# Optimization experiments

Measured on AMD Instinct MI355X. Metric: run time of the kernel, lower is better.

Reference implementation:

```python
import jax, jax.numpy as jnp
import numpy as np

H = 1000   # hidden_size
B = 64     # batch
S = 512    # encoder source length


def setup_inputs() -> dict:
    key = jax.random.key(0)
    ks = jax.random.split(key, 9)
    scale = 0.02
    return {
        "decoder_hidden": jax.random.normal(ks[0], (1, B, H), jnp.float32),
        "context": jax.random.normal(ks[1], (B, S, 2 * H), jnp.float32),
        "mask": jax.random.randint(ks[2], (B, S, 1), 0, 2) == 1,
        "W_a": jax.random.normal(ks[3], (H, 2 * H), jnp.float32) * scale,
        "W_b": jax.random.normal(ks[4], (H, H), jnp.float32) * scale,
        "W_c_w": jax.random.normal(ks[5], (1, H), jnp.float32) * scale,
        "W_c_b": jax.random.normal(ks[6], (1,), jnp.float32) * scale,
        "dense_w": jax.random.normal(ks[7], (H, 2 * H), jnp.float32) * scale,
        "dense_b": jax.random.normal(ks[8], (H,), jnp.float32) * scale,
    }


def reference(decoder_hidden, context, mask, W_a, W_b, W_c_w, W_c_b, dense_w, dense_b):
    # context_in: (B, S, H)
    context_in = jnp.einsum('bsd,hd->bsh', context, W_a)
    # hidden_in: (1, B, H) @ W_b.T -> transpose(0,1) -> (B, 1, H)
    hidden_in = jnp.transpose(jnp.einsum('nbd,hd->nbh', decoder_hidden, W_b), (1, 0, 2))
    # scores: (B, S, 1)
    attention = jnp.einsum('bsh,oh->bso', jnp.tanh(context_in + hidden_in), W_c_w) + W_c_b
    attention = jnp.where(mask, jnp.asarray(-1e6, attention.dtype), attention)
    attention_softmaxed = jax.nn.softmax(attention, axis=1)  # softmax over source length
    # weighted_sum: (B, 1, S) x (B, S, 2H) -> (B, 1, 2H)
    weighted_sum = jnp.einsum('bso,bsd->bod', attention_softmaxed, context)
    # dense: (B, 1, H)
    return jnp.einsum('bod,hd->boh', weighted_sum, dense_w) + dense_b
```

## Files before the change

### kernel.cpp

```cpp
#include <hip/hip_runtime.h>
#include <hip/hip_bf16.h>

#define H 1000
#define B 64
#define S 512
#define D 2000
#define KP 2048
#define NP 1024
#define MP 32768
#define KS 10

typedef __attribute__((ext_vector_type(8))) short short8;
typedef __attribute__((ext_vector_type(4))) float f32x4;

__device__ inline unsigned short f2bf(float f) {
  __hip_bfloat16 h = __float2bfloat16(f);
  union { __hip_bfloat16 h; unsigned short u; } c; c.h = h;
  return c.u;
}
__device__ inline float bf2f(unsigned short u) {
  union { unsigned u; float f; } x; x.u = ((unsigned)u) << 16;
  return x.f;
}

__global__ __launch_bounds__(256) void k_dect(const float* __restrict__ dec,
                                              float* __restrict__ dec_t) {
  const int d = blockIdx.x * 4 + (threadIdx.x >> 6);
  const int b = threadIdx.x & 63;
  dec_t[d * 64 + b] = dec[b * H + d];
}

__global__ __launch_bounds__(256) void k_hidden2(const float* __restrict__ dec_t,
                                                 const float* __restrict__ Wb,
                                                 float* __restrict__ hi) {
  const int h = blockIdx.x * 4 + (threadIdx.x >> 6);
  const int lane = threadIdx.x & 63;
  const float* w = Wb + (size_t)h * H;
  float acc = 0.f;
#pragma unroll 4
  for (int d = 0; d < H; ++d) acc += w[d] * dec_t[d * 64 + lane];
  hi[lane * H + h] = acc;
}

__global__ __launch_bounds__(256) void k_hidden(const float* __restrict__ dec,
                                                const float* __restrict__ Wb,
                                                float* __restrict__ hi) {
  __shared__ float sdec[H];
  const int b = blockIdx.y;
  const int h = blockIdx.x * 4 + (threadIdx.x >> 6);
  const int lane = threadIdx.x & 63;
  for (int d = threadIdx.x; d < H; d += 256) sdec[d] = dec[b * H + d];
  __syncthreads();
  const float* w = Wb + (size_t)h * H;
  float acc = 0.f;
  for (int d = lane; d < H; d += 64) acc += w[d] * sdec[d];
  for (int o = 32; o; o >>= 1) acc += __shfl_xor(acc, o);
  if (lane == 0) hi[b * H + h] = acc;
}

__global__ __launch_bounds__(256) void k_cvt_t(const float* __restrict__ src,
                                               unsigned short* __restrict__ dst,
                                               int valid_rows) {
  __shared__ unsigned short st[2][4096];
  const int rp = blockIdx.x;
  const int tid = threadIdx.x;
  const int row = tid >> 2;
  const int kq = tid & 3;

#define CVT_BODY(T, P)                                                          \
  do {                                                                          \
    const int t = (T);                                                          \
    unsigned short v[2][8];                                                     \
    _Pragma("unroll")                                                           \
    for (int w = 0; w < 2; ++w) {                                               \
      const int r = row + w * 64;                                               \
      const int grow = rp * 128 + r;                                            \
      const int gcol = t * 32 + kq * 8;                                         \
      if (grow < valid_rows && gcol + 8 <= D) {                                 \
        const float* p = src + (size_t)grow * D + gcol;                         \
        float4 x = *(const float4*)p;                                           \
        float4 y = *(const float4*)(p + 4);                                     \
        v[w][0] = f2bf(x.x); v[w][1] = f2bf(x.y); v[w][2] = f2bf(x.z);          \
        v[w][3] = f2bf(x.w); v[w][4] = f2bf(y.x); v[w][5] = f2bf(y.y);          \
        v[w][6] = f2bf(y.z); v[w][7] = f2bf(y.w);                               \
      } else {                                                                  \
        _Pragma("unroll")                                                       \
        for (int z = 0; z < 8; ++z) v[w][z] = 0;                                \
      }                                                                         \
    }                                                                           \
    *(short8*)&st[P][(kq * 128 + row) * 8] = *(short8*)&v[0][0];                \
    *(short8*)&st[P][(kq * 128 + row + 64) * 8] = *(short8*)&v[1][0];           \
    __syncthreads();                                                            \
    unsigned short* ob = dst + ((size_t)rp * 64 + t) * 4096;                    \
    *(short8*)(ob + tid * 8) = *(short8*)&st[P][tid * 8];                       \
    *(short8*)(ob + 2048 + tid * 8) = *(short8*)&st[P][2048 + tid * 8];         \
  } while (0)

  const int t0 = blockIdx.y * 16;
  for (int tt = 0; tt < 16; tt += 2) {
    CVT_BODY(t0 + tt, 0);
    CVT_BODY(t0 + tt + 1, 1);
  }
#undef CVT_BODY
}

__global__ __launch_bounds__(256) void k_scores_fast(const unsigned short* __restrict__ ctxb,
                                                     const unsigned short* __restrict__ wab,
                                                     const float* __restrict__ hi,
                                                     const float* __restrict__ Wcw,
                                                     float* __restrict__ scores) {
  __shared__ unsigned short As[3][4096];
  __shared__ unsigned short Bs[3][4096];

  const int bid = blockIdx.x;
  const int swz = (bid & 7) * 256 + (bid >> 3);
  const int rtile = swz >> 3;
  const int ctile = swz & 7;
  const int row0 = rtile * 128;
  const int col0 = ctile * 128;

  const int tid = threadIdx.x;
  const int lane = tid & 63;
  const int wid = tid >> 6;
  const int wm = wid >> 1, wn = wid & 1;
  const int fr = lane & 15, fq = lane >> 4;

  const unsigned short* ga = ctxb + (size_t)rtile * (64 * 4096);
  const unsigned short* gb = wab + (size_t)ctile * (64 * 4096);

  f32x4 acc[4][4];
#pragma unroll
  for (int i = 0; i < 4; ++i)
#pragma unroll
    for (int j = 0; j < 4; ++j) acc[i][j] = (f32x4){0.f, 0.f, 0.f, 0.f};

#define STAGE(T, BUF)                                                                                      \
  do {                                                                                                     \
    const unsigned short* pa = ga + (size_t)(T) * 4096 + tid * 8;                                          \
    const unsigned short* pb = gb + (size_t)(T) * 4096 + tid * 8;                                          \
    __builtin_amdgcn_global_load_lds((const __attribute__((address_space(1))) unsigned int*)pa,            \
                                     (__attribute__((address_space(3))) unsigned int*)&As[BUF][tid * 8],   \
                                     16, 0, 0);                                                            \
    __builtin_amdgcn_global_load_lds((const __attribute__((address_space(1))) unsigned int*)(pa + 2048),   \
                                     (__attribute__((address_space(3))) unsigned int*)&As[BUF][tid * 8 + 2048], \
                                     16, 0, 0);                                                            \
    __builtin_amdgcn_global_load_lds((const __attribute__((address_space(1))) unsigned int*)pb,            \
                                     (__attribute__((address_space(3))) unsigned int*)&Bs[BUF][tid * 8],   \
                                     16, 0, 0);                                                            \
    __builtin_amdgcn_global_load_lds((const __attribute__((address_space(1))) unsigned int*)(pb + 2048),   \
                                     (__attribute__((address_space(3))) unsigned int*)&Bs[BUF][tid * 8 + 2048], \
                                     16, 0, 0);                                                            \
  } while (0)

  const int aoff = fq * 1024 + (wm * 64 + fr) * 8;
  const int boff = fq * 1024 + (wn * 64 + fr) * 8;

#define COMPUTE(BI)                                                                     \
  do {                                                                                  \
    short8 a[4], bb[4];                                                                 \
    _Pragma("unroll")                                                                   \
    for (int mi = 0; mi < 4; ++mi) a[mi] = *(const short8*)&As[BI][aoff + mi * 128];    \
    _Pragma("unroll")                                                                   \
    for (int ni = 0; ni < 4; ++ni) bb[ni] = *(const short8*)&Bs[BI][boff + ni * 128];   \
    __builtin_amdgcn_s_setprio(1);                                                      \
    _Pragma("unroll")                                                                   \
    for (int mi = 0; mi < 4; ++mi)                                                      \
      _Pragma("unroll")                                                                 \
      for (int ni = 0; ni < 4; ++ni)                                                    \
        acc[mi][ni] = __builtin_amdgcn_mfma_f32_16x16x32_bf16(a[mi], bb[ni], acc[mi][ni], 0, 0, 0); \
    __builtin_amdgcn_s_setprio(0);                                                      \
  } while (0)

#define ITER(T, BC, BS)                                      \
  do {                                                       \
    STAGE((T) + 2, BS);                                      \
    COMPUTE(BC);                                             \
    asm volatile("s_waitcnt vmcnt(4)" ::: "memory");         \
    __builtin_amdgcn_s_barrier();                            \
  } while (0)

  STAGE(0, 0);
  STAGE(1, 1);
  asm volatile("s_waitcnt vmcnt(4)" ::: "memory");
  __builtin_amdgcn_s_barrier();

  for (int t = 0; t < 60; t += 3) {
    ITER(t, 0, 2);
    ITER(t + 1, 1, 0);
    ITER(t + 2, 2, 1);
  }
  ITER(60, 0, 2);
  ITER(61, 1, 0);
  COMPUTE(2);
  asm volatile("s_waitcnt vmcnt(0)" ::: "memory");
  __builtin_amdgcn_s_barrier();
  COMPUTE(0);
#undef ITER
#undef STAGE
#undef COMPUTE

  const int b_idx = row0 >> 9;
  float wcv[4], hiv[4];
#pragma unroll
  for (int ni = 0; ni < 4; ++ni) {
    const int h = col0 + wn * 64 + ni * 16 + fr;
    wcv[ni] = (h < H) ? Wcw[h] : 0.f;
    hiv[ni] = (h < H) ? hi[b_idx * H + h] : 0.f;
  }
#pragma unroll
  for (int mi = 0; mi < 4; ++mi) {
#pragma unroll
    for (int r = 0; r < 4; ++r) {
      float p = 0.f;
#pragma unroll
      for (int ni = 0; ni < 4; ++ni)
        p += wcv[ni] * tanhf(acc[mi][ni][r] + hiv[ni]);
      p += __shfl_xor(p, 1);
      p += __shfl_xor(p, 2);
      p += __shfl_xor(p, 4);
      p += __shfl_xor(p, 8);
      if (fr == 0)
        atomicAdd(&scores[row0 + wm * 64 + mi * 16 + fq * 4 + r], p);
    }
  }
}

#define BM 128
#define BN 128
#define BK 32
#define NT 63
__global__ __launch_bounds__(256) void k_scores(const float* __restrict__ ctx,
                                                const float* __restrict__ Wa,
                                                const float* __restrict__ hi,
                                                const float* __restrict__ Wcw,
                                                float* __restrict__ scores) {
  __shared__ unsigned short As[2][BM][BK];
  __shared__ unsigned short Bs[2][BN][BK];

  const int bid = blockIdx.x;
  const int swz = (bid & 7) * 256 + (bid >> 3);
  const int row0 = (swz >> 3) * BM;
  const int col0 = (swz & 7) * BN;

  const int tid = threadIdx.x;
  const int lane = tid & 63;
  const int wid = tid >> 6;
  const int wm = wid >> 1;
  const int wn = wid & 1;
  const int fr = lane & 15;
  const int fq = lane >> 4;

  const int trow = tid >> 1;
  const int thalf = tid & 1;

  f32x4 acc[4][4];
#pragma unroll
  for (int i = 0; i < 4; ++i)
#pragma unroll
    for (int j = 0; j < 4; ++j) acc[i][j] = (f32x4){0.f, 0.f, 0.f, 0.f};

  const float* aptr = ctx + (size_t)(row0 + trow) * D + thalf * 16;
  const int hB = col0 + trow;
  const bool bvalid = (hB < H);
  const float* bptr = Wa + (size_t)(bvalid ? hB : 0) * D + thalf * 16;

  float4 ra[4], rb[4];

#define LOADT(T)                                                     \
  do {                                                               \
    const int base = (T) * BK + thalf * 16;                          \
    _Pragma("unroll")                                                \
    for (int q = 0; q < 4; ++q) {                                    \
      const int kk = base + q * 4;                                   \
      if (kk < D) {                                                  \
        ra[q] = *(const float4*)(aptr + (T) * BK + q * 4);           \
        if (bvalid) rb[q] = *(const float4*)(bptr + (T) * BK + q * 4); \
      }                                                              \
    }                                                                \
  } while (0)

#define CVTW(T, BUF)                                                 \
  do {                                                               \
    const int base = (T) * BK + thalf * 16;                          \
    unsigned short ta[16], tb[16];                                   \
    _Pragma("unroll")                                                \
    for (int q = 0; q < 4; ++q) {                                    \
      const int kk = base + q * 4;                                   \
      const bool v = (kk < D);                                       \
      ta[q * 4 + 0] = v ? f2bf(ra[q].x) : 0;                         \
      ta[q * 4 + 1] = v ? f2bf(ra[q].y) : 0;                         \
      ta[q * 4 + 2] = v ? f2bf(ra[q].z) : 0;                         \
      ta[q * 4 + 3] = v ? f2bf(ra[q].w) : 0;                         \
      const bool vb = v && bvalid;                                   \
      tb[q * 4 + 0] = vb ? f2bf(rb[q].x) : 0;                        \
      tb[q * 4 + 1] = vb ? f2bf(rb[q].y) : 0;                        \
      tb[q * 4 + 2] = vb ? f2bf(rb[q].z) : 0;                        \
      tb[q * 4 + 3] = vb ? f2bf(rb[q].w) : 0;                        \
    }                                                                \
    *(short8*)&As[BUF][trow][thalf * 16]     = *(short8*)&ta[0];     \
    *(short8*)&As[BUF][trow][thalf * 16 + 8] = *(short8*)&ta[8];     \
    *(short8*)&Bs[BUF][trow][thalf * 16]     = *(short8*)&tb[0];     \
    *(short8*)&Bs[BUF][trow][thalf * 16 + 8] = *(short8*)&tb[8];     \
  } while (0)

  LOADT(0);
  CVTW(0, 0);
  LOADT(1);
  __syncthreads();

  int cur = 0;
  for (int t = 0; t < NT; ++t) {
    short8 a[4], bbf[4];
#pragma unroll
    for (int mi = 0; mi < 4; ++mi)
      a[mi] = *(const short8*)&As[cur][wm * 64 + mi * 16 + fr][fq * 8];
#pragma unroll
    for (int ni = 0; ni < 4; ++ni)
      bbf[ni] = *(const short8*)&Bs[cur][wn * 64 + ni * 16 + fr][fq * 8];
#pragma unroll
    for (int mi = 0; mi < 4; ++mi)
#pragma unroll
      for (int ni = 0; ni < 4; ++ni)
        acc[mi][ni] = __builtin_amdgcn_mfma_f32_16x16x32_bf16(a[mi], bbf[ni], acc[mi][ni], 0, 0, 0);

    if (t + 1 < NT) {
      CVTW(t + 1, cur ^ 1);
      if (t + 2 < NT) LOADT(t + 2);
    }
    __syncthreads();
    cur ^= 1;
  }
#undef LOADT
#undef CVTW

  const int b_idx = row0 >> 9;
  float wcv[4], hiv[4];
#pragma unroll
  for (int ni = 0; ni < 4; ++ni) {
    const int h = col0 + wn * 64 + ni * 16 + fr;
    wcv[ni] = (h < H) ? Wcw[h] : 0.f;
    hiv[ni] = (h < H) ? hi[b_idx * H + h] : 0.f;
  }
#pragma unroll
  for (int mi = 0; mi < 4; ++mi) {
#pragma unroll
    for (int r = 0; r < 4; ++r) {
      float p = 0.f;
#pragma unroll
      for (int ni = 0; ni < 4; ++ni)
        p += wcv[ni] * tanhf(acc[mi][ni][r] + hiv[ni]);
      p += __shfl_xor(p, 1);
      p += __shfl_xor(p, 2);
      p += __shfl_xor(p, 4);
      p += __shfl_xor(p, 8);
      if (fr == 0)
        atomicAdd(&scores[row0 + wm * 64 + mi * 16 + fq * 4 + r], p);
    }
  }
}

__global__ __launch_bounds__(256) void k_softmax(const float* __restrict__ scores,
                                                 const int* __restrict__ mask,
                                                 const float* __restrict__ Wcb,
                                                 float* __restrict__ probs) {
  __shared__ float buf[S];
  __shared__ float rbuf[256];
  const int b = blockIdx.x;
  const float bias = Wcb[0];
  float mx = -3.4e38f;
  for (int s = threadIdx.x; s < S; s += 256) {
    float a = mask[b * S + s] ? -1e6f : (scores[b * S + s] + bias);
    buf[s] = a;
    mx = fmaxf(mx, a);
  }
  rbuf[threadIdx.x] = mx;
  __syncthreads();
  for (int w = 128; w > 0; w >>= 1) {
    if (threadIdx.x < w) rbuf[threadIdx.x] = fmaxf(rbuf[threadIdx.x], rbuf[threadIdx.x + w]);
    __syncthreads();
  }
  mx = rbuf[0];
  __syncthreads();
  float sum = 0.f;
  for (int s = threadIdx.x; s < S; s += 256) {
    float e = expf(buf[s] - mx);
    buf[s] = e;
    sum += e;
  }
  rbuf[threadIdx.x] = sum;
  __syncthreads();
  for (int w = 128; w > 0; w >>= 1) {
    if (threadIdx.x < w) rbuf[threadIdx.x] += rbuf[threadIdx.x + w];
    __syncthreads();
  }
  const float inv = 1.f / rbuf[0];
  for (int s = threadIdx.x; s < S; s += 256) probs[b * S + s] = buf[s] * inv;
}

__global__ __launch_bounds__(256) void k_wsum_b(const unsigned short* __restrict__ ctxb,
                                                const float* __restrict__ probs,
                                                float* __restrict__ ws2) {
  __shared__ float sp[S];
  const int t = blockIdx.x;
  const int b = blockIdx.y;
  const int tid = threadIdx.x;
  const int kq = tid >> 6;
  const int lane = tid & 63;
  for (int i = tid; i < S; i += 256) sp[i] = probs[b * S + i];
  __syncthreads();
  float acc[8];
#pragma unroll
  for (int e = 0; e < 8; ++e) acc[e] = 0.f;
#pragma unroll
  for (int rp4 = 0; rp4 < 4; ++rp4) {
    const unsigned short* chunk = ctxb + ((size_t)(b * 4 + rp4) * 64 + t) * 4096;
#pragma unroll
    for (int w = 0; w < 2; ++w) {
      const int row = lane + w * 64;
      short8 v = *(const short8*)&chunk[(kq * 128 + row) * 8];
      const float pv = sp[rp4 * 128 + row];
#pragma unroll
      for (int e = 0; e < 8; ++e) acc[e] += pv * bf2f((unsigned short)v[e]);
    }
  }
#pragma unroll
  for (int o = 32; o; o >>= 1)
#pragma unroll
    for (int e = 0; e < 8; ++e) acc[e] += __shfl_xor(acc[e], o);
  const int d0 = t * 32 + kq * 8;
  if (lane == 0 && d0 < D) {
#pragma unroll
    for (int e = 0; e < 8; ++e) ws2[(size_t)b * D + d0 + e] = acc[e];
  }
}

__global__ __launch_bounds__(256) void k_wsum(const float* __restrict__ ctx,
                                              const float* __restrict__ probs,
                                              float* __restrict__ ws2) {
  __shared__ float p[S];
  const int b = blockIdx.y;
  const int d = blockIdx.x * 256 + threadIdx.x;
  for (int s = threadIdx.x; s < S; s += 256) p[s] = probs[b * S + s];
  __syncthreads();
  if (d < D) {
    float acc = 0.f;
    for (int s = 0; s < S; ++s) acc += p[s] * ctx[(size_t)(b * S + s) * D + d];
    ws2[b * D + d] = acc;
  }
}

__global__ __launch_bounds__(256) void k_dense_part(const float* __restrict__ ws2,
                                                    const float* __restrict__ Dw,
                                                    float* __restrict__ partial) {
  __shared__ float sw[64][201];
  const int tid = threadIdx.x;
  const int ks = blockIdx.y;
  const int k0 = ks * 200;
  for (int idx = tid; idx < 64 * 200; idx += 256) {
    const int b = idx / 200, k = idx - b * 200;
    sw[b][k] = ws2[(size_t)b * D + k0 + k];
  }
  __syncthreads();
  const int h = blockIdx.x * 4 + (tid >> 6);
  const int lane = tid & 63;
  const float* wrow = Dw + (size_t)h * D + k0;
  float acc = 0.f;
#pragma unroll 8
  for (int k = 0; k < 200; ++k) acc += wrow[k] * sw[lane][k];
  partial[((size_t)ks * 64 + lane) * 1000 + h] = acc;
}

__global__ __launch_bounds__(256) void k_dense_red(const float* __restrict__ partial,
                                                   const float* __restrict__ Db,
                                                   float* __restrict__ out) {
  const int idx = blockIdx.x * 256 + threadIdx.x;
  const int h = idx % 1000;
  float acc = Db[h];
#pragma unroll
  for (int ks = 0; ks < KS; ++ks) acc += partial[(size_t)ks * 64000 + idx];
  out[idx] = acc;
}

__global__ __launch_bounds__(256) void k_dense(const float* __restrict__ ws2,
                                               const float* __restrict__ Dw,
                                               const float* __restrict__ Db,
                                               float* __restrict__ out) {
  __shared__ float v[D];
  const int b = blockIdx.y;
  const int h = blockIdx.x * 256 + threadIdx.x;
  for (int d = threadIdx.x; d < D; d += 256) v[d] = ws2[b * D + d];
  __syncthreads();
  if (h < H) {
    const float* w = Dw + (size_t)h * D;
    float acc = 0.f;
    for (int d = 0; d < D; ++d) acc += w[d] * v[d];
    out[b * H + h] = acc + Db[h];
  }
}

extern "C" void kernel_launch(void* const* d_in, const int* in_sizes, int n_in,
                              void* d_out, int out_size, void* d_ws, size_t ws_size,
                              hipStream_t stream) {
  const float* dec = (const float*)d_in[0];
  const float* ctx = (const float*)d_in[1];
  const int*   mask = (const int*)d_in[2];
  const float* Wa  = (const float*)d_in[3];
  const float* Wb  = (const float*)d_in[4];
  const float* Wcw = (const float*)d_in[5];
  const float* Wcb = (const float*)d_in[6];
  const float* Dw  = (const float*)d_in[7];
  const float* Db  = (const float*)d_in[8];
  float* out = (float*)d_out;

  float* hi     = (float*)d_ws;
  float* scores = hi + B * H;
  float* probs  = scores + B * S;
  float* ws2    = probs + B * S;
  const size_t float_words = (size_t)B * H + 2 * B * S + B * D;
  unsigned short* ctx_b = (unsigned short*)((float*)d_ws + float_words);
  unsigned short* wa_b  = ctx_b + (size_t)MP * KP;
  float* dec_t  = (float*)ctx_b;
  float* partial = (float*)ctx_b;
  const size_t need = float_words * 4 + ((size_t)MP * KP + (size_t)NP * KP) * 2;

  hipMemsetAsync(scores, 0, B * S * sizeof(float), stream);
  if (ws_size >= need) {
    k_dect<<<250, 256, 0, stream>>>(dec, dec_t);
    k_hidden2<<<250, 256, 0, stream>>>(dec_t, Wb, hi);
    k_cvt_t<<<dim3(MP / 128, 4), 256, 0, stream>>>(ctx, ctx_b, MP);
    k_cvt_t<<<dim3(NP / 128, 4), 256, 0, stream>>>(Wa, wa_b, H);
    k_scores_fast<<<2048, 256, 0, stream>>>(ctx_b, wa_b, hi, Wcw, scores);
    k_softmax<<<B, 256, 0, stream>>>(scores, mask, Wcb, probs);
    k_wsum_b<<<dim3(63, B), 256, 0, stream>>>(ctx_b, probs, ws2);
    k_dense_part<<<dim3(250, KS), 256, 0, stream>>>(ws2, Dw, partial);
    k_dense_red<<<250, 256, 0, stream>>>(partial, Db, out);
  } else {
    k_hidden<<<dim3(250, B), 256, 0, stream>>>(dec, Wb, hi);
    k_scores<<<2048, 256, 0, stream>>>(ctx, Wa, hi, Wcw, scores);
    k_softmax<<<B, 256, 0, stream>>>(scores, mask, Wcb, probs);
    k_wsum<<<dim3((D + 255) / 256, B), 256, 0, stream>>>(ctx, probs, ws2);
    k_dense<<<dim3((H + 255) / 256, B), 256, 0, stream>>>(ws2, Dw, Db, out);
  }
}
```

Before: 462.3 us.

## Enlarge scores GEMM tiles to 256x256 with 32x32 MFMA and fast tanh

The scores GEMM moves from 128x128 tiles with 4 waves to 256x256 tiles with 8 waves, using 32x32x16 bf16 MFMA instructions. The bf16 packed layout of context and W_a changes to 256-row chunks to match, and the conversion and weighted-sum kernels are updated to read it. This raises arithmetic intensity and reduces redundant global and LDS traffic per FLOP. It also swaps tanhf for an exp-based tanh. The cost is much larger LDS use (96KB) and more registers per thread, which lowers occupancy, and there are fewer blocks (512) to fill the CUs.

```diff
diff --git a/kernel.cpp b/kernel.cpp
--- a/kernel.cpp
+++ b/kernel.cpp
@@ -12,6 +12,7 @@
 
 typedef __attribute__((ext_vector_type(8))) short short8;
 typedef __attribute__((ext_vector_type(4))) float f32x4;
+typedef __attribute__((ext_vector_type(16))) float f32x16;
 
 __device__ inline unsigned short f2bf(float f) {
   __hip_bfloat16 h = __float2bfloat16(f);
@@ -21,6 +22,10 @@
 __device__ inline float bf2f(unsigned short u) {
   union { unsigned u; float f; } x; x.u = ((unsigned)u) << 16;
   return x.f;
+}
+__device__ inline float tanh_fast(float x) {
+  float e2 = __expf(2.f * x);
+  return 1.f - 2.f / (e2 + 1.f);
 }
 
 __global__ __launch_bounds__(256) void k_dect(const float* __restrict__ dec,
@@ -61,20 +66,19 @@
 __global__ __launch_bounds__(256) void k_cvt_t(const float* __restrict__ src,
                                                unsigned short* __restrict__ dst,
                                                int valid_rows) {
-  __shared__ unsigned short st[2][4096];
+  __shared__ unsigned short st[2][8192];
   const int rp = blockIdx.x;
   const int tid = threadIdx.x;
-  const int row = tid >> 2;
+  const int r0 = tid >> 2;
   const int kq = tid & 3;
 
 #define CVT_BODY(T, P)                                                          \
   do {                                                                          \
     const int t = (T);                                                          \
-    unsigned short v[2][8];                                                     \
+    unsigned short v[4][8];                                                     \
     _Pragma("unroll")                                                           \
-    for (int w = 0; w < 2; ++w) {                                               \
-      const int r = row + w * 64;                                               \
-      const int grow = rp * 128 + r;                                            \
+    for (int w = 0; w < 4; ++w) {                                               \
+      const int grow = rp * 256 + r0 + w * 64;                                  \
       const int gcol = t * 32 + kq * 8;                                         \
       if (grow < valid_rows && gcol + 8 <= D) {                                 \
         const float* p = src + (size_t)grow * D + gcol;                         \
@@ -88,87 +92,98 @@
         for (int z = 0; z < 8; ++z) v[w][z] = 0;                                \
       }                                                                         \
     }                                                                           \
-    *(short8*)&st[P][(kq * 128 + row) * 8] = *(short8*)&v[0][0];                \
-    *(short8*)&st[P][(kq * 128 + row + 64) * 8] = *(short8*)&v[1][0];           \
+    _Pragma("unroll")                                                           \
+    for (int w = 0; w < 4; ++w)                                                 \
+      *(short8*)&st[P][(kq * 256 + r0 + w * 64) * 8] = *(short8*)&v[w][0];      \
     __syncthreads();                                                            \
-    unsigned short* ob = dst + ((size_t)rp * 64 + t) * 4096;                    \
-    *(short8*)(ob + tid * 8) = *(short8*)&st[P][tid * 8];                       \
-    *(short8*)(ob + 2048 + tid * 8) = *(short8*)&st[P][2048 + tid * 8];         \
+    unsigned short* ob = dst + ((size_t)rp * 64 + t) * 8192;                    \
+    _Pragma("unroll")                                                           \
+    for (int s = 0; s < 4; ++s)                                                 \
+      *(short8*)(ob + (tid + s * 256) * 8) = *(short8*)&st[P][(tid + s * 256) * 8]; \
   } while (0)
 
-  const int t0 = blockIdx.y * 16;
-  for (int tt = 0; tt < 16; tt += 2) {
+  const int t0 = blockIdx.y * 8;
+  for (int tt = 0; tt < 8; tt += 2) {
     CVT_BODY(t0 + tt, 0);
     CVT_BODY(t0 + tt + 1, 1);
   }
 #undef CVT_BODY
 }
 
-__global__ __launch_bounds__(256) void k_scores_fast(const unsigned short* __restrict__ ctxb,
+__global__ __launch_bounds__(512) void k_scores_fast(const unsigned short* __restrict__ ctxb,
                                                      const unsigned short* __restrict__ wab,
                                                      const float* __restrict__ hi,
                                                      const float* __restrict__ Wcw,
                                                      float* __restrict__ scores) {
-  __shared__ unsigned short As[3][4096];
-  __shared__ unsigned short Bs[3][4096];
+  __shared__ unsigned short As[3][8192];
+  __shared__ unsigned short Bs[3][8192];
 
   const int bid = blockIdx.x;
-  const int swz = (bid & 7) * 256 + (bid >> 3);
-  const int rtile = swz >> 3;
-  const int ctile = swz & 7;
-  const int row0 = rtile * 128;
-  const int col0 = ctile * 128;
+  const int swz = (bid & 7) * 64 + (bid >> 3);
+  const int rtile = swz >> 2;
+  const int ctile = swz & 3;
+  const int row0 = rtile * 256;
+  const int col0 = ctile * 256;
 
   const int tid = threadIdx.x;
   const int lane = tid & 63;
   const int wid = tid >> 6;
-  const int wm = wid >> 1, wn = wid & 1;
-  const int fr = lane & 15, fq = lane >> 4;
-
-  const unsigned short* ga = ctxb + (size_t)rtile * (64 * 4096);
-  const unsigned short* gb = wab + (size_t)ctile * (64 * 4096);
-
-  f32x4 acc[4][4];
+  const int wm = wid >> 2;
+  const int wn = wid & 3;
+  const int ln31 = lane & 31;
+  const int kh = lane >> 5;
+
+  const unsigned short* ga = ctxb + (size_t)rtile * (64 * 8192);
+  const unsigned short* gb = wab + (size_t)ctile * (64 * 8192);
+
+  f32x16 acc[4][2];
 #pragma unroll
   for (int i = 0; i < 4; ++i)
 #pragma unroll
-    for (int j = 0; j < 4; ++j) acc[i][j] = (f32x4){0.f, 0.f, 0.f, 0.f};
+    for (int j = 0; j < 2; ++j)
+#pragma unroll
+      for (int r = 0; r < 16; ++r) acc[i][j][r] = 0.f;
 
 #define STAGE(T, BUF)                                                                                      \
   do {                                                                                                     \
-    const unsigned short* pa = ga + (size_t)(T) * 4096 + tid * 8;                                          \
-    const unsigned short* pb = gb + (size_t)(T) * 4096 + tid * 8;                                          \
+    const unsigned short* pa = ga + (size_t)(T) * 8192 + tid * 8;                                          \
+    const unsigned short* pb = gb + (size_t)(T) * 8192 + tid * 8;                                          \
     __builtin_amdgcn_global_load_lds((const __attribute__((address_space(1))) unsigned int*)pa,            \
                                      (__attribute__((address_space(3))) unsigned int*)&As[BUF][tid * 8],   \
                                      16, 0, 0);                                                            \
-    __builtin_amdgcn_global_load_lds((const __attribute__((address_space(1))) unsigned int*)(pa + 2048),   \
-                                     (__attribute__((address_space(3))) unsigned int*)&As[BUF][tid * 8 + 2048], \
+    __builtin_amdgcn_global_load_lds((const __attribute__((address_space(1))) unsigned int*)(pa + 4096),   \
+                                     (__attribute__((address_space(3))) unsigned int*)&As[BUF][tid * 8 + 4096], \
                                      16, 0, 0);                                                            \
     __builtin_amdgcn_global_load_lds((const __attribute__((address_space(1))) unsigned int*)pb,            \
                                      (__attribute__((address_space(3))) unsigned int*)&Bs[BUF][tid * 8],   \
                                      16, 0, 0);                                                            \
-    __builtin_amdgcn_global_load_lds((const __attribute__((address_space(1))) unsigned int*)(pb + 2048),   \
-                                     (__attribute__((address_space(3))) unsigned int*)&Bs[BUF][tid * 8 + 2048], \
+    __builtin_amdgcn_global_load_lds((const __attribute__((address_space(1))) unsigned int*)(pb + 4096),   \
+                                     (__attribute__((address_space(3))) unsigned int*)&Bs[BUF][tid * 8 + 4096], \
                                      16, 0, 0);                                                            \
   } while (0)
 
-  const int aoff = fq * 1024 + (wm * 64 + fr) * 8;
-  const int boff = fq * 1024 + (wn * 64 + fr) * 8;
+  const int abase = kh * 2048 + (wm * 128 + ln31) * 8;
+  const int bbase = kh * 2048 + (wn * 64 + ln31) * 8;
 
 #define COMPUTE(BI)                                                                     \
   do {                                                                                  \
-    short8 a[4], bb[4];                                                                 \
     _Pragma("unroll")                                                                   \
-    for (int mi = 0; mi < 4; ++mi) a[mi] = *(const short8*)&As[BI][aoff + mi * 128];    \
-    _Pragma("unroll")                                                                   \
-    for (int ni = 0; ni < 4; ++ni) bb[ni] = *(const short8*)&Bs[BI][boff + ni * 128];   \
-    __builtin_amdgcn_s_setprio(1);                                                      \
-    _Pragma("unroll")                                                                   \
-    for (int mi = 0; mi < 4; ++mi)                                                      \
+    for (int ks = 0; ks < 2; ++ks) {                                                    \
+      short8 a[4], bb[2];                                                               \
       _Pragma("unroll")                                                                 \
-      for (int ni = 0; ni < 4; ++ni)                                                    \
-        acc[mi][ni] = __builtin_amdgcn_mfma_f32_16x16x32_bf16(a[mi], bb[ni], acc[mi][ni], 0, 0, 0); \
-    __builtin_amdgcn_s_setprio(0);                                                      \
+      for (int mi = 0; mi < 4; ++mi)                                                    \
+        a[mi] = *(const short8*)&As[BI][abase + ks * 4096 + mi * 256];                  \
+      _Pragma("unroll")                                                                 \
+      for (int ni = 0; ni < 2; ++ni)                                                    \
+        bb[ni] = *(const short8*)&Bs[BI][bbase + ks * 4096 + ni * 256];                 \
+      __builtin_amdgcn_s_setprio(1);                                                    \
+      _Pragma("unroll")                                                                 \
+      for (int mi = 0; mi < 4; ++mi)                                                    \
+        _Pragma("unroll")                                                               \
+        for (int ni = 0; ni < 2; ++ni)                                                  \
+          acc[mi][ni] = __builtin_amdgcn_mfma_f32_32x32x16_bf16(a[mi], bb[ni], acc[mi][ni], 0, 0, 0); \
+      __builtin_amdgcn_s_setprio(0);                                                    \
+    }                                                                                   \
   } while (0)
 
 #define ITER(T, BC, BS)                                      \
@@ -200,27 +215,28 @@
 #undef COMPUTE
 
   const int b_idx = row0 >> 9;
-  float wcv[4], hiv[4];
-#pragma unroll
-  for (int ni = 0; ni < 4; ++ni) {
-    const int h = col0 + wn * 64 + ni * 16 + fr;
-    wcv[ni] = (h < H) ? Wcw[h] : 0.f;
-    hiv[ni] = (h < H) ? hi[b_idx * H + h] : 0.f;
+  float wc[2], hv[2];
+#pragma unroll
+  for (int ni = 0; ni < 2; ++ni) {
+    const int h = col0 + wn * 64 + ni * 32 + ln31;
+    wc[ni] = (h < H) ? Wcw[h] : 0.f;
+    hv[ni] = (h < H) ? hi[b_idx * H + h] : 0.f;
   }
 #pragma unroll
   for (int mi = 0; mi < 4; ++mi) {
 #pragma unroll
-    for (int r = 0; r < 4; ++r) {
-      float p = 0.f;
-#pragma unroll
-      for (int ni = 0; ni < 4; ++ni)
-        p += wcv[ni] * tanhf(acc[mi][ni][r] + hiv[ni]);
+    for (int reg = 0; reg < 16; ++reg) {
+      float p = wc[0] * tanh_fast(acc[mi][0][reg] + hv[0])
+              + wc[1] * tanh_fast(acc[mi][1][reg] + hv[1]);
       p += __shfl_xor(p, 1);
       p += __shfl_xor(p, 2);
       p += __shfl_xor(p, 4);
       p += __shfl_xor(p, 8);
-      if (fr == 0)
-        atomicAdd(&scores[row0 + wm * 64 + mi * 16 + fq * 4 + r], p);
+      p += __shfl_xor(p, 16);
+      if (ln31 == 0) {
+        const int n = row0 + wm * 128 + mi * 32 + (reg & 3) + 8 * (reg >> 2) + 4 * kh;
+        atomicAdd(&scores[n], p);
+      }
     }
   }
 }
@@ -404,7 +420,7 @@
   const int t = blockIdx.x;
   const int b = blockIdx.y;
   const int tid = threadIdx.x;
-  const int kq = tid >> 6;
+  const int p = tid >> 6;
   const int lane = tid & 63;
   for (int i = tid; i < S; i += 256) sp[i] = probs[b * S + i];
   __syncthreads();
@@ -412,13 +428,13 @@
 #pragma unroll
   for (int e = 0; e < 8; ++e) acc[e] = 0.f;
 #pragma unroll
-  for (int rp4 = 0; rp4 < 4; ++rp4) {
-    const unsigned short* chunk = ctxb + ((size_t)(b * 4 + rp4) * 64 + t) * 4096;
-#pragma unroll
-    for (int w = 0; w < 2; ++w) {
-      const int row = lane + w * 64;
-      short8 v = *(const short8*)&chunk[(kq * 128 + row) * 8];
-      const float pv = sp[rp4 * 128 + row];
+  for (int rt = 0; rt < 2; ++rt) {
+    const unsigned short* chunk = ctxb + ((size_t)(b * 2 + rt) * 64 + t) * 8192;
+#pragma unroll
+    for (int half = 0; half < 4; ++half) {
+      const int row = half * 64 + lane;
+      short8 v = *(const short8*)&chunk[(p * 256 + row) * 8];
+      const float pv = sp[rt * 256 + row];
 #pragma unroll
       for (int e = 0; e < 8; ++e) acc[e] += pv * bf2f((unsigned short)v[e]);
     }
@@ -427,7 +443,7 @@
   for (int o = 32; o; o >>= 1)
 #pragma unroll
     for (int e = 0; e < 8; ++e) acc[e] += __shfl_xor(acc[e], o);
-  const int d0 = t * 32 + kq * 8;
+  const int d0 = t * 32 + p * 8;
   if (lane == 0 && d0 < D) {
 #pragma unroll
     for (int e = 0; e < 8; ++e) ws2[(size_t)b * D + d0 + e] = acc[e];
@@ -527,9 +543,9 @@
   if (ws_size >= need) {
     k_dect<<<250, 256, 0, stream>>>(dec, dec_t);
     k_hidden2<<<250, 256, 0, stream>>>(dec_t, Wb, hi);
-    k_cvt_t<<<dim3(MP / 128, 4), 256, 0, stream>>>(ctx, ctx_b, MP);
-    k_cvt_t<<<dim3(NP / 128, 4), 256, 0, stream>>>(Wa, wa_b, H);
-    k_scores_fast<<<2048, 256, 0, stream>>>(ctx_b, wa_b, hi, Wcw, scores);
+    k_cvt_t<<<dim3(MP / 256, 8), 256, 0, stream>>>(ctx, ctx_b, MP);
+    k_cvt_t<<<dim3(NP / 256, 8), 256, 0, stream>>>(Wa, wa_b, H);
+    k_scores_fast<<<512, 512, 0, stream>>>(ctx_b, wa_b, hi, Wcw, scores);
     k_softmax<<<B, 256, 0, stream>>>(scores, mask, Wcb, probs);
     k_wsum_b<<<dim3(63, B), 256, 0, stream>>>(ctx_b, probs, ws2);
     k_dense_part<<<dim3(250, KS), 256, 0, stream>>>(ws2, Dw, partial);
```

Result: faster. 408.5 us (-11.6%).
